# Kernel tuning notes

Measured on AMD Instinct MI355X. Metric: run time of the kernel, lower is better.

The kernel has to match this reference:

```python
import jax, jax.numpy as jnp
import numpy as np

N = 100000   # nodes
E = 1200000  # edges
B = 128      # graphs per batch
F = 92       # raw node features
D = 64       # pre_hidden_size == gc_dim == post_hidden_size
L = 3        # n_gcn
Z = 2 * D + 1  # CGConv concat width


def setup_inputs() -> dict:
    key = jax.random.key(0)
    ks = jax.random.split(key, 24)
    s = 0.1
    inp = {
        "X": jax.random.normal(ks[0], (N, F), jnp.float32),
        "edge_idx": jax.random.randint(ks[1], (2, E), 0, N),
        "edge_weight": jax.random.uniform(ks[2], (E,), jnp.float32),
        "edge_attr": jax.random.normal(ks[3], (E,), jnp.float32),
        "batch_map": jnp.sort(jax.random.randint(ks[4], (N,), 0, B)),
        # pre-GCN MLP: F->D, D->D, D->D, relu after each
        "pre_W0": jax.random.normal(ks[5], (F, D)) * s,
        "pre_b0": jnp.zeros((D,), jnp.float32),
        "pre_W1": jax.random.normal(ks[6], (D, D)) * s,
        "pre_b1": jnp.zeros((D,), jnp.float32),
        "pre_W2": jax.random.normal(ks[7], (D, D)) * s,
        "pre_b2": jnp.zeros((D,), jnp.float32),
        # CGConv gates: lin_f / lin_s: (2D+1)->D, stacked over L layers
        "cg_Wf": jax.random.normal(ks[8], (L, Z, D)) * s,
        "cg_bf": jnp.zeros((L, D), jnp.float32),
        "cg_Ws": jax.random.normal(ks[9], (L, Z, D)) * s,
        "cg_bs": jnp.zeros((L, D), jnp.float32),
        # post-GCN MLP: D->D x3 (relu) then D->1
        "post_W0": jax.random.normal(ks[10], (D, D)) * s,
        "post_b0": jnp.zeros((D,), jnp.float32),
        "post_W1": jax.random.normal(ks[11], (D, D)) * s,
        "post_b1": jnp.zeros((D,), jnp.float32),
        "post_W2": jax.random.normal(ks[12], (D, D)) * s,
        "post_b2": jnp.zeros((D,), jnp.float32),
        "post_Wf": jax.random.normal(ks[13], (D, 1)) * s,
        "post_bf": jnp.zeros((1,), jnp.float32),
    }
    return inp


def _forward(X, edge_idx, edge_weight, edge_attr, batch_map,
             pre_W0, pre_b0, pre_W1, pre_b1, pre_W2, pre_b2,
             cg_Wf, cg_bf, cg_Ws, cg_bs,
             post_W0, post_b0, post_W1, post_b1, post_W2, post_b2,
             post_Wf, post_bf):
    relu = jax.nn.relu
    # pre-GC MLP
    h = relu(X @ pre_W0 + pre_b0)
    h = relu(h @ pre_W1 + pre_b1)
    h = relu(h @ pre_W2 + pre_b2)  # [N, D]

    src = edge_idx[0]  # x_j (message source)
    dst = edge_idx[1]  # x_i (aggregation target)
    ea = edge_attr.reshape(-1, 1)  # [E, 1]
    # in-degree for mean aggregation (nodes with no edges -> 0 via denom clamp)
    deg = jax.ops.segment_sum(jnp.ones((E,), h.dtype), dst, num_segments=N)
    denom = jnp.maximum(deg, 1.0)[:, None]  # [N, 1]

    for l in range(L):
        # CGConv: z = [x_i || x_j || e], out = x + mean_i(sigmoid(z Wf) * softplus(z Ws))
        z = jnp.concatenate([h[dst], h[src], ea], axis=-1)  # [E, 2D+1]
        m = jax.nn.sigmoid(z @ cg_Wf[l] + cg_bf[l]) * jax.nn.softplus(z @ cg_Ws[l] + cg_bs[l])
        agg = jax.ops.segment_sum(m, dst, num_segments=N) / denom
        h = relu(h + agg)  # residual + activation from pyg Sequential

    # early global mean pool per graph
    gsum = jax.ops.segment_sum(h, batch_map, num_segments=B)
    gcnt = jax.ops.segment_sum(jnp.ones((N,), h.dtype), batch_map, num_segments=B)
    g = gsum / jnp.maximum(gcnt, 1.0)[:, None]  # [B, D]

    # post-GC MLP
    g = relu(g @ post_W0 + post_b0)
    g = relu(g @ post_W1 + post_b1)
    g = relu(g @ post_W2 + post_b2)
    return g @ post_Wf + post_bf  # [B, 1]


def reference(X, edge_idx, edge_weight, edge_attr, batch_map,
              pre_W0, pre_b0, pre_W1, pre_b1, pre_W2, pre_b2,
              cg_Wf, cg_bf, cg_Ws, cg_bs,
              post_W0, post_b0, post_W1, post_b1, post_W2, post_b2,
              post_Wf, post_bf):
    return _forward(X, edge_idx, edge_weight, edge_attr, batch_map,
                    pre_W0, pre_b0, pre_W1, pre_b1, pre_W2, pre_b2,
                    cg_Wf, cg_bf, cg_Ws, cg_bs,
                    post_W0, post_b0, post_W1, post_b1, post_W2, post_b2,
                    post_Wf, post_bf)
```

## Files before the change

### kernel.cpp

```cpp
#include <hip/hip_runtime.h>
#include <hip/hip_bf16.h>
#include <math.h>

#define GN 100000
#define GE 1200000
#define GB 128
#define GF 92
#define GD 64
#define GL 3
#define GZ 129

__device__ __forceinline__ unsigned int f2bf_rne(float x)
{
    unsigned int u = __float_as_uint(x);
    u += 0x7fffu + ((u >> 16) & 1u);
    return u >> 16;
}

__global__ __launch_bounds__(256, 2) void premlp_kernel(
    const float* __restrict__ X,
    const float* __restrict__ W0, const float* __restrict__ b0,
    const float* __restrict__ W1, const float* __restrict__ b1,
    const float* __restrict__ W2, const float* __restrict__ b2,
    const float* __restrict__ WfD, const float* __restrict__ WsD,
    const float* __restrict__ WfS, const float* __restrict__ WsS,
    const float* __restrict__ bf, const float* __restrict__ bs,
    float* __restrict__ hout, unsigned int* __restrict__ Pout,
    float* __restrict__ Qout, int N)
{
    __shared__ __align__(16) float Wl[8192];
    const int tid = threadIdx.x;
    const int n = blockIdx.x * 256 + tid;
    const int nn = (n < N) ? n : (N - 1);
    const bool act = (n < N);

    float acc[64], accS[64];

    {
        const float4* __restrict__ s4 = (const float4*)W0;
        float4* __restrict__ d4 = (float4*)Wl;
        for (int i = tid; i < 1472; i += 256) d4[i] = s4[i];
    }
    __syncthreads();

#pragma unroll
    for (int j = 0; j < 64; ++j) acc[j] = b0[j];
    {
        const float4* __restrict__ row4 = (const float4*)(X + (size_t)nn * GF);
#pragma unroll 2
        for (int c = 0; c < 23; ++c) {
            float4 v = row4[c];
            const float* __restrict__ w = Wl + c * 256;
#pragma unroll
            for (int j = 0; j < 64; ++j) {
                acc[j] = fmaf(v.x, w[j], acc[j]);
                acc[j] = fmaf(v.y, w[64 + j], acc[j]);
                acc[j] = fmaf(v.z, w[128 + j], acc[j]);
                acc[j] = fmaf(v.w, w[192 + j], acc[j]);
            }
        }
    }
    if (act) {
        float4* __restrict__ op = (float4*)(hout + (size_t)n * 64);
#pragma unroll
        for (int q = 0; q < 16; ++q)
            op[q] = make_float4(fmaxf(acc[q * 4], 0.f), fmaxf(acc[q * 4 + 1], 0.f),
                                fmaxf(acc[q * 4 + 2], 0.f), fmaxf(acc[q * 4 + 3], 0.f));
    }

    __syncthreads();
    {
        const float4* __restrict__ s4 = (const float4*)W1;
        float4* __restrict__ d4 = (float4*)Wl;
        for (int i = tid; i < 1024; i += 256) d4[i] = s4[i];
    }
    __syncthreads();

#pragma unroll
    for (int j = 0; j < 64; ++j) acc[j] = b1[j];
    {
        const float4* __restrict__ row4 = (const float4*)(hout + (size_t)nn * 64);
#pragma unroll 2
        for (int c = 0; c < 16; ++c) {
            float4 v = row4[c];
            const float* __restrict__ w = Wl + c * 256;
#pragma unroll
            for (int j = 0; j < 64; ++j) {
                acc[j] = fmaf(v.x, w[j], acc[j]);
                acc[j] = fmaf(v.y, w[64 + j], acc[j]);
                acc[j] = fmaf(v.z, w[128 + j], acc[j]);
                acc[j] = fmaf(v.w, w[192 + j], acc[j]);
            }
        }
    }
    if (act) {
        float4* __restrict__ op = (float4*)(hout + (size_t)n * 64);
#pragma unroll
        for (int q = 0; q < 16; ++q)
            op[q] = make_float4(fmaxf(acc[q * 4], 0.f), fmaxf(acc[q * 4 + 1], 0.f),
                                fmaxf(acc[q * 4 + 2], 0.f), fmaxf(acc[q * 4 + 3], 0.f));
    }

    __syncthreads();
    {
        const float4* __restrict__ s4 = (const float4*)W2;
        float4* __restrict__ d4 = (float4*)Wl;
        for (int i = tid; i < 1024; i += 256) d4[i] = s4[i];
    }
    __syncthreads();

#pragma unroll
    for (int j = 0; j < 64; ++j) acc[j] = b2[j];
    {
        const float4* __restrict__ row4 = (const float4*)(hout + (size_t)nn * 64);
#pragma unroll 2
        for (int c = 0; c < 16; ++c) {
            float4 v = row4[c];
            const float* __restrict__ w = Wl + c * 256;
#pragma unroll
            for (int j = 0; j < 64; ++j) {
                acc[j] = fmaf(v.x, w[j], acc[j]);
                acc[j] = fmaf(v.y, w[64 + j], acc[j]);
                acc[j] = fmaf(v.z, w[128 + j], acc[j]);
                acc[j] = fmaf(v.w, w[192 + j], acc[j]);
            }
        }
    }
    if (act) {
        float4* __restrict__ op = (float4*)(hout + (size_t)n * 64);
#pragma unroll
        for (int q = 0; q < 16; ++q)
            op[q] = make_float4(fmaxf(acc[q * 4], 0.f), fmaxf(acc[q * 4 + 1], 0.f),
                                fmaxf(acc[q * 4 + 2], 0.f), fmaxf(acc[q * 4 + 3], 0.f));
    }

    __syncthreads();
    {
        const float4* __restrict__ s4 = (const float4*)WfS;
        const float4* __restrict__ t4 = (const float4*)WsS;
        float4* __restrict__ d4 = (float4*)Wl;
        for (int i = tid; i < 1024; i += 256) {
            d4[i] = s4[i];
            d4[1024 + i] = t4[i];
        }
    }
    __syncthreads();

#pragma unroll
    for (int j = 0; j < 64; ++j) { acc[j] = 0.f; accS[j] = 0.f; }
    {
        const float4* __restrict__ row4 = (const float4*)(hout + (size_t)nn * 64);
#pragma unroll 2
        for (int c = 0; c < 16; ++c) {
            float4 v = row4[c];
            const float* __restrict__ wf = Wl + c * 256;
            const float* __restrict__ ws = Wl + 4096 + c * 256;
#pragma unroll
            for (int j = 0; j < 64; ++j) {
                acc[j] = fmaf(v.x, wf[j], acc[j]);
                acc[j] = fmaf(v.y, wf[64 + j], acc[j]);
                acc[j] = fmaf(v.z, wf[128 + j], acc[j]);
                acc[j] = fmaf(v.w, wf[192 + j], acc[j]);
                accS[j] = fmaf(v.x, ws[j], accS[j]);
                accS[j] = fmaf(v.y, ws[64 + j], accS[j]);
                accS[j] = fmaf(v.z, ws[128 + j], accS[j]);
                accS[j] = fmaf(v.w, ws[192 + j], accS[j]);
            }
        }
    }
    if (act) {
        uint4* __restrict__ pp = (uint4*)(Pout + (size_t)n * 64);
#pragma unroll
        for (int q = 0; q < 16; ++q) {
            uint4 pk;
            pk.x = f2bf_rne(acc[q * 4])     | (f2bf_rne(accS[q * 4]) << 16);
            pk.y = f2bf_rne(acc[q * 4 + 1]) | (f2bf_rne(accS[q * 4 + 1]) << 16);
            pk.z = f2bf_rne(acc[q * 4 + 2]) | (f2bf_rne(accS[q * 4 + 2]) << 16);
            pk.w = f2bf_rne(acc[q * 4 + 3]) | (f2bf_rne(accS[q * 4 + 3]) << 16);
            pp[q] = pk;
        }
    }

    __syncthreads();
    {
        const float4* __restrict__ s4 = (const float4*)WfD;
        const float4* __restrict__ t4 = (const float4*)WsD;
        float4* __restrict__ d4 = (float4*)Wl;
        for (int i = tid; i < 1024; i += 256) {
            d4[i] = s4[i];
            d4[1024 + i] = t4[i];
        }
    }
    __syncthreads();

#pragma unroll
    for (int j = 0; j < 64; ++j) { acc[j] = bf[j]; accS[j] = bs[j]; }
    {
        const float4* __restrict__ row4 = (const float4*)(hout + (size_t)nn * 64);
#pragma unroll 2
        for (int c = 0; c < 16; ++c) {
            float4 v = row4[c];
            const float* __restrict__ wf = Wl + c * 256;
            const float* __restrict__ ws = Wl + 4096 + c * 256;
#pragma unroll
            for (int j = 0; j < 64; ++j) {
                acc[j] = fmaf(v.x, wf[j], acc[j]);
                acc[j] = fmaf(v.y, wf[64 + j], acc[j]);
                acc[j] = fmaf(v.z, wf[128 + j], acc[j]);
                acc[j] = fmaf(v.w, wf[192 + j], acc[j]);
                accS[j] = fmaf(v.x, ws[j], accS[j]);
                accS[j] = fmaf(v.y, ws[64 + j], accS[j]);
                accS[j] = fmaf(v.z, ws[128 + j], accS[j]);
                accS[j] = fmaf(v.w, ws[192 + j], accS[j]);
            }
        }
    }
    if (act) {
        float4* __restrict__ qp = (float4*)(Qout + (size_t)n * 128);
#pragma unroll
        for (int q = 0; q < 32; ++q)
            qp[q] = make_float4(acc[q * 2], accS[q * 2], acc[q * 2 + 1], accS[q * 2 + 1]);
    }
}

__global__ __launch_bounds__(256, 2) void pjq_kernel(
    const float* __restrict__ h,
    const float* __restrict__ Wf, const float* __restrict__ Ws,
    const float* __restrict__ bfv, const float* __restrict__ bsv,
    unsigned int* __restrict__ P, float* __restrict__ Q, int N)
{
    __shared__ __align__(16) float Wl[8192];
    const int tid = threadIdx.x;
    const int n = blockIdx.x * 256 + tid;
    const int nn = (n < N) ? n : (N - 1);
    const bool act = (n < N);

    float aF[64], aS[64];

    {
        const float4* __restrict__ s4 = (const float4*)(Wf + 64 * 64);
        const float4* __restrict__ t4 = (const float4*)(Ws + 64 * 64);
        float4* __restrict__ d4 = (float4*)Wl;
        for (int i = tid; i < 1024; i += 256) {
            d4[i] = s4[i];
            d4[1024 + i] = t4[i];
        }
    }
    __syncthreads();

#pragma unroll
    for (int j = 0; j < 64; ++j) { aF[j] = 0.f; aS[j] = 0.f; }
    {
        const float4* __restrict__ row4 = (const float4*)(h + (size_t)nn * 64);
#pragma unroll 2
        for (int c = 0; c < 16; ++c) {
            float4 v = row4[c];
            const float* __restrict__ wf = Wl + c * 256;
            const float* __restrict__ ws = Wl + 4096 + c * 256;
#pragma unroll
            for (int j = 0; j < 64; ++j) {
                aF[j] = fmaf(v.x, wf[j], aF[j]);
                aF[j] = fmaf(v.y, wf[64 + j], aF[j]);
                aF[j] = fmaf(v.z, wf[128 + j], aF[j]);
                aF[j] = fmaf(v.w, wf[192 + j], aF[j]);
                aS[j] = fmaf(v.x, ws[j], aS[j]);
                aS[j] = fmaf(v.y, ws[64 + j], aS[j]);
                aS[j] = fmaf(v.z, ws[128 + j], aS[j]);
                aS[j] = fmaf(v.w, ws[192 + j], aS[j]);
            }
        }
    }
    if (act) {
        uint4* __restrict__ pp = (uint4*)(P + (size_t)n * 64);
#pragma unroll
        for (int q = 0; q < 16; ++q) {
            uint4 pk;
            pk.x = f2bf_rne(aF[q * 4])     | (f2bf_rne(aS[q * 4]) << 16);
            pk.y = f2bf_rne(aF[q * 4 + 1]) | (f2bf_rne(aS[q * 4 + 1]) << 16);
            pk.z = f2bf_rne(aF[q * 4 + 2]) | (f2bf_rne(aS[q * 4 + 2]) << 16);
            pk.w = f2bf_rne(aF[q * 4 + 3]) | (f2bf_rne(aS[q * 4 + 3]) << 16);
            pp[q] = pk;
        }
    }

    __syncthreads();
    {
        const float4* __restrict__ s4 = (const float4*)Wf;
        const float4* __restrict__ t4 = (const float4*)Ws;
        float4* __restrict__ d4 = (float4*)Wl;
        for (int i = tid; i < 1024; i += 256) {
            d4[i] = s4[i];
            d4[1024 + i] = t4[i];
        }
    }
    __syncthreads();

#pragma unroll
    for (int j = 0; j < 64; ++j) { aF[j] = bfv[j]; aS[j] = bsv[j]; }
    {
        const float4* __restrict__ row4 = (const float4*)(h + (size_t)nn * 64);
#pragma unroll 2
        for (int c = 0; c < 16; ++c) {
            float4 v = row4[c];
            const float* __restrict__ wf = Wl + c * 256;
            const float* __restrict__ ws = Wl + 4096 + c * 256;
#pragma unroll
            for (int j = 0; j < 64; ++j) {
                aF[j] = fmaf(v.x, wf[j], aF[j]);
                aF[j] = fmaf(v.y, wf[64 + j], aF[j]);
                aF[j] = fmaf(v.z, wf[128 + j], aF[j]);
                aF[j] = fmaf(v.w, wf[192 + j], aF[j]);
                aS[j] = fmaf(v.x, ws[j], aS[j]);
                aS[j] = fmaf(v.y, ws[64 + j], aS[j]);
                aS[j] = fmaf(v.z, ws[128 + j], aS[j]);
                aS[j] = fmaf(v.w, ws[192 + j], aS[j]);
            }
        }
    }
    if (act) {
        float4* __restrict__ qp = (float4*)(Q + (size_t)n * 128);
#pragma unroll
        for (int q = 0; q < 32; ++q)
            qp[q] = make_float4(aF[q * 2], aS[q * 2], aF[q * 2 + 1], aS[q * 2 + 1]);
    }
}

__global__ __launch_bounds__(256) void deg_kernel(
    const int* __restrict__ dst, int* __restrict__ deg, int E)
{
    int e = blockIdx.x * blockDim.x + threadIdx.x;
    if (e < E) atomicAdd(&deg[dst[e]], 1);
}

__global__ __launch_bounds__(1024) void scanA_kernel(
    const int* __restrict__ deg, int* __restrict__ iscan,
    int* __restrict__ bsum, int N)
{
    __shared__ int lds[1024];
    int tid = threadIdx.x;
    int gid = blockIdx.x * 1024 + tid;
    int v = (gid < N) ? deg[gid] : 0;
    lds[tid] = v; __syncthreads();
    for (int off = 1; off < 1024; off <<= 1) {
        int t = (tid >= off) ? lds[tid - off] : 0;
        __syncthreads();
        lds[tid] += t;
        __syncthreads();
    }
    if (gid < N) iscan[gid] = lds[tid];
    if (tid == 1023) bsum[blockIdx.x] = lds[1023];
}

__global__ __launch_bounds__(128) void scanB_kernel(
    const int* __restrict__ bsum, int* __restrict__ boff, int nb)
{
    __shared__ int lds[128];
    int t = threadIdx.x;
    int v = (t < nb) ? bsum[t] : 0;
    lds[t] = v; __syncthreads();
    for (int off = 1; off < 128; off <<= 1) {
        int u = (t >= off) ? lds[t - off] : 0;
        __syncthreads();
        lds[t] += u;
        __syncthreads();
    }
    if (t < nb) boff[t] = lds[t] - v;
}

__global__ __launch_bounds__(256) void scanC_kernel(
    const int* __restrict__ iscan, const int* __restrict__ boff,
    const int* __restrict__ deg,
    int* __restrict__ rowptr, int* __restrict__ cursor, int N)
{
    int i = blockIdx.x * blockDim.x + threadIdx.x;
    if (i >= N) return;
    int incl = iscan[i] + boff[i >> 10];
    rowptr[i + 1] = incl;
    cursor[i] = incl - deg[i];
    if (i == 0) rowptr[0] = 0;
}

__global__ __launch_bounds__(256) void escatter_kernel(
    const int* __restrict__ src, const int* __restrict__ dst,
    const float* __restrict__ ea, int* __restrict__ cursor,
    int2* __restrict__ e_se, int E)
{
    int e = blockIdx.x * blockDim.x + threadIdx.x;
    if (e >= E) return;
    int pos = atomicAdd(&cursor[dst[e]], 1);
    e_se[pos] = make_int2(src[e], __float_as_int(ea[e]));
}

__global__ __launch_bounds__(256) void edge_kernel(
    const float* __restrict__ h, const int* __restrict__ rowptr,
    const int2* __restrict__ e_se,
    const unsigned int* __restrict__ P,
    const float* __restrict__ Q,
    const float* __restrict__ Wf, const float* __restrict__ Ws,
    float* __restrict__ hout)
{
    int n = blockIdx.x * 4 + (threadIdx.x >> 6);
    int d = threadIdx.x & 63;

    const float2 qv = ((const float2*)Q)[(size_t)n * 64 + d];
    float qf = qv.x, qs = qv.y;
    float wf = Wf[128 * 64 + d];
    float ws = Ws[128 * 64 + d];

    size_t idx = (size_t)n * 64 + d;
    float hres = h[idx];

    int rb = rowptr[n], re = rowptr[n + 1];
    float agg = 0.f;
#pragma unroll 8
    for (int p = rb; p < re; ++p) {
        int2 se = e_se[p];
        int s = se.x;
        float ea = __int_as_float(se.y);
        unsigned int pv = P[(size_t)s * 64 + d];
        float pf = __uint_as_float(pv << 16);
        float psv = __uint_as_float(pv & 0xffff0000u);
        float xF = fmaf(ea, wf, qf + pf);
        float xS = fmaf(ea, ws, qs + psv);
        float sig = __builtin_amdgcn_rcpf(1.f + __expf(-xF));
        float t = __expf(-fabsf(xS));
        float sp = fmaxf(xS, 0.f) + __logf(1.f + t);
        agg = fmaf(sig, sp, agg);
    }

    float inv = 1.f / (float)max(re - rb, 1);
    hout[idx] = fmaxf(hres + agg * inv, 0.f);
}

__global__ __launch_bounds__(256) void gstart_kernel(
    const int* __restrict__ bm, int* __restrict__ gstart, int N)
{
    int i = blockIdx.x * blockDim.x + threadIdx.x;
    if (i >= N) return;
    int b = bm[i];
    int prev = (i == 0) ? -1 : bm[i - 1];
    for (int g = prev + 1; g <= b; ++g) gstart[g] = i;
    if (i == N - 1)
        for (int g = b + 1; g <= GB; ++g) gstart[g] = N;
}

__global__ __launch_bounds__(256) void pool_seg_kernel(
    const float* __restrict__ h, const int* __restrict__ gstart,
    float* __restrict__ g)
{
    int b = blockIdx.x;
    int s = gstart[b], e = gstart[b + 1];
    int d = threadIdx.x & 63;
    int w = threadIdx.x >> 6;
    float acc = 0.f;
    for (int n = s + w; n < e; n += 4)
        acc += h[(size_t)n * 64 + d];
    __shared__ float lds[256];
    lds[threadIdx.x] = acc;
    __syncthreads();
    if (w == 0) {
        acc = lds[d] + lds[64 + d] + lds[128 + d] + lds[192 + d];
        g[b * 64 + d] = acc / fmaxf((float)(e - s), 1.f);
    }
}

__global__ __launch_bounds__(256) void postmlp_kernel(
    const float* __restrict__ g,
    const float* __restrict__ W0, const float* __restrict__ b0,
    const float* __restrict__ W1, const float* __restrict__ b1,
    const float* __restrict__ W2, const float* __restrict__ b2,
    const float* __restrict__ Wfin, const float* __restrict__ bfin,
    float* __restrict__ out)
{
    int b = blockIdx.x * 4 + (threadIdx.x >> 6);
    int d = threadIdx.x & 63;
    float h = g[(size_t)b * 64 + d];

    float acc = b0[d];
#pragma unroll
    for (int k = 0; k < 64; ++k)
        acc = fmaf(__shfl(h, k, 64), W0[k * 64 + d], acc);
    h = fmaxf(acc, 0.f);

    acc = b1[d];
#pragma unroll
    for (int k = 0; k < 64; ++k)
        acc = fmaf(__shfl(h, k, 64), W1[k * 64 + d], acc);
    h = fmaxf(acc, 0.f);

    acc = b2[d];
#pragma unroll
    for (int k = 0; k < 64; ++k)
        acc = fmaf(__shfl(h, k, 64), W2[k * 64 + d], acc);
    h = fmaxf(acc, 0.f);

    float v = h * Wfin[d];
#pragma unroll
    for (int off = 32; off >= 1; off >>= 1)
        v += __shfl_xor(v, off, 64);
    if (d == 0) out[b] = v + bfin[0];
}

extern "C" void kernel_launch(void* const* d_in, const int* in_sizes, int n_in,
                              void* d_out, int out_size, void* d_ws, size_t ws_size,
                              hipStream_t stream)
{
    const float* X      = (const float*)d_in[0];
    const int*   eidx   = (const int*)d_in[1];
    const float* ea     = (const float*)d_in[3];
    const int*   bm     = (const int*)d_in[4];
    const float* pre_W0 = (const float*)d_in[5];
    const float* pre_b0 = (const float*)d_in[6];
    const float* pre_W1 = (const float*)d_in[7];
    const float* pre_b1 = (const float*)d_in[8];
    const float* pre_W2 = (const float*)d_in[9];
    const float* pre_b2 = (const float*)d_in[10];
    const float* cg_Wf  = (const float*)d_in[11];
    const float* cg_bf  = (const float*)d_in[12];
    const float* cg_Ws  = (const float*)d_in[13];
    const float* cg_bs  = (const float*)d_in[14];
    const float* post_W0 = (const float*)d_in[15];
    const float* post_b0 = (const float*)d_in[16];
    const float* post_W1 = (const float*)d_in[17];
    const float* post_b1 = (const float*)d_in[18];
    const float* post_W2 = (const float*)d_in[19];
    const float* post_b2 = (const float*)d_in[20];
    const float* post_Wf = (const float*)d_in[21];
    const float* post_bf = (const float*)d_in[22];

    const int* src = eidx;
    const int* dst = eidx + GE;

    const size_t N64 = (size_t)GN * 64;
    float* hA    = (float*)d_ws;
    float* hB    = hA + N64;
    unsigned int* P = (unsigned int*)(hB + N64);
    int* deg_i   = (int*)(P + N64);
    int* iscan   = deg_i + GN;
    int* bsum    = iscan + GN;
    int* boff    = bsum + 128;
    int* rowptr  = boff + 128;
    int* cursor  = rowptr + GN + 2;
    int2* e_se   = (int2*)(cursor + GN);
    int* gstart  = (int*)(e_se + GE);
    float* g0    = (float*)(gstart + GB + 1);
    float* Q     = g0 + (size_t)GB * 64;

    const int TPB = 256;
    int gridE  = (GE + TPB - 1) / TPB;
    int gridN  = (GN + TPB - 1) / TPB;
    int gridND = ((GN * 64) + TPB - 1) / TPB;
    int scanBlocks = (GN + 1023) / 1024;

    const float* Wf0 = cg_Wf;
    const float* Ws0 = cg_Ws;
    const float* Wf1 = cg_Wf + (size_t)1 * GZ * GD;
    const float* Ws1 = cg_Ws + (size_t)1 * GZ * GD;
    const float* Wf2 = cg_Wf + (size_t)2 * GZ * GD;
    const float* Ws2 = cg_Ws + (size_t)2 * GZ * GD;

    premlp_kernel<<<gridN, TPB, 0, stream>>>(
        X, pre_W0, pre_b0, pre_W1, pre_b1, pre_W2, pre_b2,
        Wf0, Ws0, Wf0 + 64 * 64, Ws0 + 64 * 64, cg_bf, cg_bs,
        hA, P, Q, GN);

    hipMemsetAsync(deg_i, 0, GN * sizeof(int), stream);
    deg_kernel<<<gridE, TPB, 0, stream>>>(dst, deg_i, GE);
    scanA_kernel<<<scanBlocks, 1024, 0, stream>>>(deg_i, iscan, bsum, GN);
    scanB_kernel<<<1, 128, 0, stream>>>(bsum, boff, scanBlocks);
    scanC_kernel<<<gridN, TPB, 0, stream>>>(iscan, boff, deg_i, rowptr, cursor, GN);
    escatter_kernel<<<gridE, TPB, 0, stream>>>(src, dst, ea, cursor, e_se, GE);

    gstart_kernel<<<gridN, TPB, 0, stream>>>(bm, gstart, GN);

    edge_kernel<<<gridND, TPB, 0, stream>>>(
        hA, rowptr, e_se, P, Q, Wf0, Ws0, hB);
    pjq_kernel<<<gridN, TPB, 0, stream>>>(
        hB, Wf1, Ws1, cg_bf + GD, cg_bs + GD, P, Q, GN);
    edge_kernel<<<gridND, TPB, 0, stream>>>(
        hB, rowptr, e_se, P, Q, Wf1, Ws1, hA);
    pjq_kernel<<<gridN, TPB, 0, stream>>>(
        hA, Wf2, Ws2, cg_bf + 2 * GD, cg_bs + 2 * GD, P, Q, GN);
    edge_kernel<<<gridND, TPB, 0, stream>>>(
        hA, rowptr, e_se, P, Q, Wf2, Ws2, hB);

    pool_seg_kernel<<<GB, TPB, 0, stream>>>(hB, gstart, g0);

    postmlp_kernel<<<GB / 4, TPB, 0, stream>>>(
        g0, post_W0, post_b0, post_W1, post_b1, post_W2, post_b2,
        post_Wf, post_bf, (float*)d_out);
}
```

Baseline: 983.7 us.

## Split node MLP columns across four waves and stage hidden rows in LDS

The pre-MLP and per-layer projection kernels now assign 64 nodes per block, with each of four wavefronts computing 16 output columns instead of one thread computing all 64. Intermediate hidden activations are kept in a padded shared-memory tile rather than round-tripping through global memory, and the paired Wf/Ws projections are done sequentially with one weight matrix in LDS at a time. This cuts per-thread accumulator registers from 128 to 32 so occupancy can rise (launch bounds raised to 4 blocks). The cost is more barriers, more LDS traffic, and four times as many blocks. The WfS/WsS argument swap is offset by a matching swap at the call site.

```diff
diff --git a/kernel.cpp b/kernel.cpp
--- a/kernel.cpp
+++ b/kernel.cpp
@@ -10,6 +10,8 @@
 #define GL 3
 #define GZ 129
 
+#define HS 65
+
 __device__ __forceinline__ unsigned int f2bf_rne(float x)
 {
     unsigned int u = __float_as_uint(x);
@@ -17,24 +19,28 @@
     return u >> 16;
 }
 
-__global__ __launch_bounds__(256, 2) void premlp_kernel(
+__global__ __launch_bounds__(256, 4) void premlp_kernel(
     const float* __restrict__ X,
     const float* __restrict__ W0, const float* __restrict__ b0,
     const float* __restrict__ W1, const float* __restrict__ b1,
     const float* __restrict__ W2, const float* __restrict__ b2,
     const float* __restrict__ WfD, const float* __restrict__ WsD,
-    const float* __restrict__ WfS, const float* __restrict__ WsS,
+    const float* __restrict__ WsS, const float* __restrict__ WfS,
     const float* __restrict__ bf, const float* __restrict__ bs,
     float* __restrict__ hout, unsigned int* __restrict__ Pout,
     float* __restrict__ Qout, int N)
 {
-    __shared__ __align__(16) float Wl[8192];
+    __shared__ __align__(16) float Wl[5888];
+    __shared__ float hl[64 * HS];
     const int tid = threadIdx.x;
-    const int n = blockIdx.x * 256 + tid;
+    const int lane = tid & 63;
+    const int col0 = (tid >> 6) * 16;
+    const int base = blockIdx.x * 64;
+    const int n = base + lane;
     const int nn = (n < N) ? n : (N - 1);
     const bool act = (n < N);
 
-    float acc[64], accS[64];
+    float acc[16], acc2[16];
 
     {
         const float4* __restrict__ s4 = (const float4*)W0;
@@ -44,15 +50,14 @@
     __syncthreads();
 
 #pragma unroll
-    for (int j = 0; j < 64; ++j) acc[j] = b0[j];
+    for (int j = 0; j < 16; ++j) acc[j] = b0[col0 + j];
     {
         const float4* __restrict__ row4 = (const float4*)(X + (size_t)nn * GF);
-#pragma unroll 2
         for (int c = 0; c < 23; ++c) {
             float4 v = row4[c];
-            const float* __restrict__ w = Wl + c * 256;
-#pragma unroll
-            for (int j = 0; j < 64; ++j) {
+            const float* __restrict__ w = Wl + c * 256 + col0;
+#pragma unroll
+            for (int j = 0; j < 16; ++j) {
                 acc[j] = fmaf(v.x, w[j], acc[j]);
                 acc[j] = fmaf(v.y, w[64 + j], acc[j]);
                 acc[j] = fmaf(v.z, w[128 + j], acc[j]);
@@ -60,268 +65,319 @@
             }
         }
     }
+    __syncthreads();
+#pragma unroll
+    for (int j = 0; j < 16; ++j) hl[lane * HS + col0 + j] = fmaxf(acc[j], 0.f);
+    {
+        const float4* __restrict__ s4 = (const float4*)W1;
+        float4* __restrict__ d4 = (float4*)Wl;
+        for (int i = tid; i < 1024; i += 256) d4[i] = s4[i];
+    }
+    __syncthreads();
+
+#pragma unroll
+    for (int j = 0; j < 16; ++j) acc[j] = b1[col0 + j];
+    for (int c = 0; c < 16; ++c) {
+        float h0 = hl[lane * HS + 4 * c + 0];
+        float h1 = hl[lane * HS + 4 * c + 1];
+        float h2 = hl[lane * HS + 4 * c + 2];
+        float h3 = hl[lane * HS + 4 * c + 3];
+        const float* __restrict__ w = Wl + c * 256 + col0;
+#pragma unroll
+        for (int j = 0; j < 16; ++j) {
+            acc[j] = fmaf(h0, w[j], acc[j]);
+            acc[j] = fmaf(h1, w[64 + j], acc[j]);
+            acc[j] = fmaf(h2, w[128 + j], acc[j]);
+            acc[j] = fmaf(h3, w[192 + j], acc[j]);
+        }
+    }
+    __syncthreads();
+#pragma unroll
+    for (int j = 0; j < 16; ++j) hl[lane * HS + col0 + j] = fmaxf(acc[j], 0.f);
+    {
+        const float4* __restrict__ s4 = (const float4*)W2;
+        float4* __restrict__ d4 = (float4*)Wl;
+        for (int i = tid; i < 1024; i += 256) d4[i] = s4[i];
+    }
+    __syncthreads();
+
+#pragma unroll
+    for (int j = 0; j < 16; ++j) acc[j] = b2[col0 + j];
+    for (int c = 0; c < 16; ++c) {
+        float h0 = hl[lane * HS + 4 * c + 0];
+        float h1 = hl[lane * HS + 4 * c + 1];
+        float h2 = hl[lane * HS + 4 * c + 2];
+        float h3 = hl[lane * HS + 4 * c + 3];
+        const float* __restrict__ w = Wl + c * 256 + col0;
+#pragma unroll
+        for (int j = 0; j < 16; ++j) {
+            acc[j] = fmaf(h0, w[j], acc[j]);
+            acc[j] = fmaf(h1, w[64 + j], acc[j]);
+            acc[j] = fmaf(h2, w[128 + j], acc[j]);
+            acc[j] = fmaf(h3, w[192 + j], acc[j]);
+        }
+    }
+    __syncthreads();
+#pragma unroll
+    for (int j = 0; j < 16; ++j) hl[lane * HS + col0 + j] = fmaxf(acc[j], 0.f);
     if (act) {
-        float4* __restrict__ op = (float4*)(hout + (size_t)n * 64);
-#pragma unroll
-        for (int q = 0; q < 16; ++q)
+        float4* __restrict__ op = (float4*)(hout + (size_t)n * 64 + col0);
+#pragma unroll
+        for (int q = 0; q < 4; ++q)
             op[q] = make_float4(fmaxf(acc[q * 4], 0.f), fmaxf(acc[q * 4 + 1], 0.f),
                                 fmaxf(acc[q * 4 + 2], 0.f), fmaxf(acc[q * 4 + 3], 0.f));
     }
-
-    __syncthreads();
-    {
-        const float4* __restrict__ s4 = (const float4*)W1;
-        float4* __restrict__ d4 = (float4*)Wl;
-        for (int i = tid; i < 1024; i += 256) d4[i] = s4[i];
-    }
-    __syncthreads();
-
-#pragma unroll
-    for (int j = 0; j < 64; ++j) acc[j] = b1[j];
-    {
-        const float4* __restrict__ row4 = (const float4*)(hout + (size_t)nn * 64);
-#pragma unroll 2
-        for (int c = 0; c < 16; ++c) {
-            float4 v = row4[c];
-            const float* __restrict__ w = Wl + c * 256;
-#pragma unroll
-            for (int j = 0; j < 64; ++j) {
-                acc[j] = fmaf(v.x, w[j], acc[j]);
-                acc[j] = fmaf(v.y, w[64 + j], acc[j]);
-                acc[j] = fmaf(v.z, w[128 + j], acc[j]);
-                acc[j] = fmaf(v.w, w[192 + j], acc[j]);
-            }
+    {
+        const float4* __restrict__ s4 = (const float4*)WfS;
+        float4* __restrict__ d4 = (float4*)Wl;
+        for (int i = tid; i < 1024; i += 256) d4[i] = s4[i];
+    }
+    __syncthreads();
+
+#pragma unroll
+    for (int j = 0; j < 16; ++j) acc[j] = 0.f;
+    for (int c = 0; c < 16; ++c) {
+        float h0 = hl[lane * HS + 4 * c + 0];
+        float h1 = hl[lane * HS + 4 * c + 1];
+        float h2 = hl[lane * HS + 4 * c + 2];
+        float h3 = hl[lane * HS + 4 * c + 3];
+        const float* __restrict__ w = Wl + c * 256 + col0;
+#pragma unroll
+        for (int j = 0; j < 16; ++j) {
+            acc[j] = fmaf(h0, w[j], acc[j]);
+            acc[j] = fmaf(h1, w[64 + j], acc[j]);
+            acc[j] = fmaf(h2, w[128 + j], acc[j]);
+            acc[j] = fmaf(h3, w[192 + j], acc[j]);
+        }
+    }
+    __syncthreads();
+    {
+        const float4* __restrict__ s4 = (const float4*)WsS;
+        float4* __restrict__ d4 = (float4*)Wl;
+        for (int i = tid; i < 1024; i += 256) d4[i] = s4[i];
+    }
+    __syncthreads();
+
+#pragma unroll
+    for (int j = 0; j < 16; ++j) acc2[j] = 0.f;
+    for (int c = 0; c < 16; ++c) {
+        float h0 = hl[lane * HS + 4 * c + 0];
+        float h1 = hl[lane * HS + 4 * c + 1];
+        float h2 = hl[lane * HS + 4 * c + 2];
+        float h3 = hl[lane * HS + 4 * c + 3];
+        const float* __restrict__ w = Wl + c * 256 + col0;
+#pragma unroll
+        for (int j = 0; j < 16; ++j) {
+            acc2[j] = fmaf(h0, w[j], acc2[j]);
+            acc2[j] = fmaf(h1, w[64 + j], acc2[j]);
+            acc2[j] = fmaf(h2, w[128 + j], acc2[j]);
+            acc2[j] = fmaf(h3, w[192 + j], acc2[j]);
         }
     }
     if (act) {
-        float4* __restrict__ op = (float4*)(hout + (size_t)n * 64);
-#pragma unroll
-        for (int q = 0; q < 16; ++q)
-            op[q] = make_float4(fmaxf(acc[q * 4], 0.f), fmaxf(acc[q * 4 + 1], 0.f),
-                                fmaxf(acc[q * 4 + 2], 0.f), fmaxf(acc[q * 4 + 3], 0.f));
-    }
-
-    __syncthreads();
-    {
-        const float4* __restrict__ s4 = (const float4*)W2;
-        float4* __restrict__ d4 = (float4*)Wl;
-        for (int i = tid; i < 1024; i += 256) d4[i] = s4[i];
-    }
-    __syncthreads();
-
-#pragma unroll
-    for (int j = 0; j < 64; ++j) acc[j] = b2[j];
-    {
-        const float4* __restrict__ row4 = (const float4*)(hout + (size_t)nn * 64);
-#pragma unroll 2
-        for (int c = 0; c < 16; ++c) {
-            float4 v = row4[c];
-            const float* __restrict__ w = Wl + c * 256;
-#pragma unroll
-            for (int j = 0; j < 64; ++j) {
-                acc[j] = fmaf(v.x, w[j], acc[j]);
-                acc[j] = fmaf(v.y, w[64 + j], acc[j]);
-                acc[j] = fmaf(v.z, w[128 + j], acc[j]);
-                acc[j] = fmaf(v.w, w[192 + j], acc[j]);
-            }
+        uint4* __restrict__ pp = (uint4*)(Pout + (size_t)n * 64 + col0);
+#pragma unroll
+        for (int q = 0; q < 4; ++q) {
+            uint4 pk;
+            pk.x = f2bf_rne(acc[q * 4])     | (f2bf_rne(acc2[q * 4]) << 16);
+            pk.y = f2bf_rne(acc[q * 4 + 1]) | (f2bf_rne(acc2[q * 4 + 1]) << 16);
+            pk.z = f2bf_rne(acc[q * 4 + 2]) | (f2bf_rne(acc2[q * 4 + 2]) << 16);
+            pk.w = f2bf_rne(acc[q * 4 + 3]) | (f2bf_rne(acc2[q * 4 + 3]) << 16);
+            pp[q] = pk;
+        }
+    }
+    __syncthreads();
+    {
+        const float4* __restrict__ s4 = (const float4*)WfD;
+        float4* __restrict__ d4 = (float4*)Wl;
+        for (int i = tid; i < 1024; i += 256) d4[i] = s4[i];
+    }
+    __syncthreads();
+
+#pragma unroll
+    for (int j = 0; j < 16; ++j) acc[j] = bf[col0 + j];
+    for (int c = 0; c < 16; ++c) {
+        float h0 = hl[lane * HS + 4 * c + 0];
+        float h1 = hl[lane * HS + 4 * c + 1];
+        float h2 = hl[lane * HS + 4 * c + 2];
+        float h3 = hl[lane * HS + 4 * c + 3];
+        const float* __restrict__ w = Wl + c * 256 + col0;
+#pragma unroll
+        for (int j = 0; j < 16; ++j) {
+            acc[j] = fmaf(h0, w[j], acc[j]);
+            acc[j] = fmaf(h1, w[64 + j], acc[j]);
+            acc[j] = fmaf(h2, w[128 + j], acc[j]);
+            acc[j] = fmaf(h3, w[192 + j], acc[j]);
+        }
+    }
+    __syncthreads();
+    {
+        const float4* __restrict__ s4 = (const float4*)WsD;
+        float4* __restrict__ d4 = (float4*)Wl;
+        for (int i = tid; i < 1024; i += 256) d4[i] = s4[i];
+    }
+    __syncthreads();
+
+#pragma unroll
+    for (int j = 0; j < 16; ++j) acc2[j] = bs[col0 + j];
+    for (int c = 0; c < 16; ++c) {
+        float h0 = hl[lane * HS + 4 * c + 0];
+        float h1 = hl[lane * HS + 4 * c + 1];
+        float h2 = hl[lane * HS + 4 * c + 2];
+        float h3 = hl[lane * HS + 4 * c + 3];
+        const float* __restrict__ w = Wl + c * 256 + col0;
+#pragma unroll
+        for (int j = 0; j < 16; ++j) {
+            acc2[j] = fmaf(h0, w[j], acc2[j]);
+            acc2[j] = fmaf(h1, w[64 + j], acc2[j]);
+            acc2[j] = fmaf(h2, w[128 + j], acc2[j]);
+            acc2[j] = fmaf(h3, w[192 + j], acc2[j]);
         }
     }
     if (act) {
-        float4* __restrict__ op = (float4*)(hout + (size_t)n * 64);
-#pragma unroll
-        for (int q = 0; q < 16; ++q)
-            op[q] = make_float4(fmaxf(acc[q * 4], 0.f), fmaxf(acc[q * 4 + 1], 0.f),
-                                fmaxf(acc[q * 4 + 2], 0.f), fmaxf(acc[q * 4 + 3], 0.f));
-    }
-
-    __syncthreads();
-    {
-        const float4* __restrict__ s4 = (const float4*)WfS;
-        const float4* __restrict__ t4 = (const float4*)WsS;
-        float4* __restrict__ d4 = (float4*)Wl;
-        for (int i = tid; i < 1024; i += 256) {
-            d4[i] = s4[i];
-            d4[1024 + i] = t4[i];
-        }
-    }
-    __syncthreads();
-
-#pragma unroll
-    for (int j = 0; j < 64; ++j) { acc[j] = 0.f; accS[j] = 0.f; }
-    {
-        const float4* __restrict__ row4 = (const float4*)(hout + (size_t)nn * 64);
-#pragma unroll 2
-        for (int c = 0; c < 16; ++c) {
-            float4 v = row4[c];
-            const float* __restrict__ wf = Wl + c * 256;
-            const float* __restrict__ ws = Wl + 4096 + c * 256;
-#pragma unroll
-            for (int j = 0; j < 64; ++j) {
-                acc[j] = fmaf(v.x, wf[j], acc[j]);
-                acc[j] = fmaf(v.y, wf[64 + j], acc[j]);
-                acc[j] = fmaf(v.z, wf[128 + j], acc[j]);
-                acc[j] = fmaf(v.w, wf[192 + j], acc[j]);
-                accS[j] = fmaf(v.x, ws[j], accS[j]);
-                accS[j] = fmaf(v.y, ws[64 + j], accS[j]);
-                accS[j] = fmaf(v.z, ws[128 + j], accS[j]);
-                accS[j] = fmaf(v.w, ws[192 + j], accS[j]);
-            }
-        }
-    }
-    if (act) {
-        uint4* __restrict__ pp = (uint4*)(Pout + (size_t)n * 64);
-#pragma unroll
-        for (int q = 0; q < 16; ++q) {
-            uint4 pk;
-            pk.x = f2bf_rne(acc[q * 4])     | (f2bf_rne(accS[q * 4]) << 16);
-            pk.y = f2bf_rne(acc[q * 4 + 1]) | (f2bf_rne(accS[q * 4 + 1]) << 16);
-            pk.z = f2bf_rne(acc[q * 4 + 2]) | (f2bf_rne(accS[q * 4 + 2]) << 16);
-            pk.w = f2bf_rne(acc[q * 4 + 3]) | (f2bf_rne(accS[q * 4 + 3]) << 16);
-            pp[q] = pk;
-        }
-    }
-
-    __syncthreads();
-    {
-        const float4* __restrict__ s4 = (const float4*)WfD;
-        const float4* __restrict__ t4 = (const float4*)WsD;
-        float4* __restrict__ d4 = (float4*)Wl;
-        for (int i = tid; i < 1024; i += 256) {
-            d4[i] = s4[i];
-            d4[1024 + i] = t4[i];
-        }
-    }
-    __syncthreads();
-
-#pragma unroll
-    for (int j = 0; j < 64; ++j) { acc[j] = bf[j]; accS[j] = bs[j]; }
-    {
-        const float4* __restrict__ row4 = (const float4*)(hout + (size_t)nn * 64);
-#pragma unroll 2
-        for (int c = 0; c < 16; ++c) {
-            float4 v = row4[c];
-            const float* __restrict__ wf = Wl + c * 256;
-            const float* __restrict__ ws = Wl + 4096 + c * 256;
-#pragma unroll
-            for (int j = 0; j < 64; ++j) {
-                acc[j] = fmaf(v.x, wf[j], acc[j]);
-                acc[j] = fmaf(v.y, wf[64 + j], acc[j]);
-                acc[j] = fmaf(v.z, wf[128 + j], acc[j]);
-                acc[j] = fmaf(v.w, wf[192 + j], acc[j]);
-                accS[j] = fmaf(v.x, ws[j], accS[j]);
-                accS[j] = fmaf(v.y, ws[64 + j], accS[j]);
-                accS[j] = fmaf(v.z, ws[128 + j], accS[j]);
-                accS[j] = fmaf(v.w, ws[192 + j], accS[j]);
-            }
-        }
-    }
-    if (act) {
-        float4* __restrict__ qp = (float4*)(Qout + (size_t)n * 128);
-#pragma unroll
-        for (int q = 0; q < 32; ++q)
-            qp[q] = make_float4(acc[q * 2], accS[q * 2], acc[q * 2 + 1], accS[q * 2 + 1]);
-    }
-}
-
-__global__ __launch_bounds__(256, 2) void pjq_kernel(
+        float4* __restrict__ qp = (float4*)(Qout + (size_t)n * 128 + col0 * 2);
+#pragma unroll
+        for (int q = 0; q < 8; ++q)
+            qp[q] = make_float4(acc[q * 2], acc2[q * 2], acc[q * 2 + 1], acc2[q * 2 + 1]);
+    }
+}
+
+__global__ __launch_bounds__(256, 4) void pjq_kernel(
     const float* __restrict__ h,
     const float* __restrict__ Wf, const float* __restrict__ Ws,
     const float* __restrict__ bfv, const float* __restrict__ bsv,
     unsigned int* __restrict__ P, float* __restrict__ Q, int N)
 {
-    __shared__ __align__(16) float Wl[8192];
+    __shared__ __align__(16) float Wl[4096];
+    __shared__ float hl[64 * HS];
     const int tid = threadIdx.x;
-    const int n = blockIdx.x * 256 + tid;
-    const int nn = (n < N) ? n : (N - 1);
+    const int lane = tid & 63;
+    const int col0 = (tid >> 6) * 16;
+    const int base = blockIdx.x * 64;
+    const int n = base + lane;
     const bool act = (n < N);
 
-    float aF[64], aS[64];
-
+    float acc[16], acc2[16];
+
+    for (int q = tid; q < 1024; q += 256) {
+        int r = q >> 4, c4 = q & 15;
+        int rr = base + r; rr = (rr < N) ? rr : (N - 1);
+        float4 v = ((const float4*)(h + (size_t)rr * 64))[c4];
+        float* dp = hl + r * HS + c4 * 4;
+        dp[0] = v.x; dp[1] = v.y; dp[2] = v.z; dp[3] = v.w;
+    }
     {
         const float4* __restrict__ s4 = (const float4*)(Wf + 64 * 64);
-        const float4* __restrict__ t4 = (const float4*)(Ws + 64 * 64);
-        float4* __restrict__ d4 = (float4*)Wl;
-        for (int i = tid; i < 1024; i += 256) {
-            d4[i] = s4[i];
-            d4[1024 + i] = t4[i];
-        }
-    }
-    __syncthreads();
-
-#pragma unroll
-    for (int j = 0; j < 64; ++j) { aF[j] = 0.f; aS[j] = 0.f; }
-    {
-        const float4* __restrict__ row4 = (const float4*)(h + (size_t)nn * 64);
-#pragma unroll 2
-        for (int c = 0; c < 16; ++c) {
-            float4 v = row4[c];
-            const float* __restrict__ wf = Wl + c * 256;
-            const float* __restrict__ ws = Wl + 4096 + c * 256;
-#pragma unroll
-            for (int j = 0; j < 64; ++j) {
-                aF[j] = fmaf(v.x, wf[j], aF[j]);
-                aF[j] = fmaf(v.y, wf[64 + j], aF[j]);
-                aF[j] = fmaf(v.z, wf[128 + j], aF[j]);
-                aF[j] = fmaf(v.w, wf[192 + j], aF[j]);
-                aS[j] = fmaf(v.x, ws[j], aS[j]);
-                aS[j] = fmaf(v.y, ws[64 + j], aS[j]);
-                aS[j] = fmaf(v.z, ws[128 + j], aS[j]);
-                aS[j] = fmaf(v.w, ws[192 + j], aS[j]);
-            }
+        float4* __restrict__ d4 = (float4*)Wl;
+        for (int i = tid; i < 1024; i += 256) d4[i] = s4[i];
+    }
+    __syncthreads();
+
+#pragma unroll
+    for (int j = 0; j < 16; ++j) acc[j] = 0.f;
+    for (int c = 0; c < 16; ++c) {
+        float h0 = hl[lane * HS + 4 * c + 0];
+        float h1 = hl[lane * HS + 4 * c + 1];
+        float h2 = hl[lane * HS + 4 * c + 2];
+        float h3 = hl[lane * HS + 4 * c + 3];
+        const float* __restrict__ w = Wl + c * 256 + col0;
+#pragma unroll
+        for (int j = 0; j < 16; ++j) {
+            acc[j] = fmaf(h0, w[j], acc[j]);
+            acc[j] = fmaf(h1, w[64 + j], acc[j]);
+            acc[j] = fmaf(h2, w[128 + j], acc[j]);
+            acc[j] = fmaf(h3, w[192 + j], acc[j]);
+        }
+    }
+    __syncthreads();
+    {
+        const float4* __restrict__ s4 = (const float4*)(Ws + 64 * 64);
+        float4* __restrict__ d4 = (float4*)Wl;
+        for (int i = tid; i < 1024; i += 256) d4[i] = s4[i];
+    }
+    __syncthreads();
+
+#pragma unroll
+    for (int j = 0; j < 16; ++j) acc2[j] = 0.f;
+    for (int c = 0; c < 16; ++c) {
+        float h0 = hl[lane * HS + 4 * c + 0];
+        float h1 = hl[lane * HS + 4 * c + 1];
+        float h2 = hl[lane * HS + 4 * c + 2];
+        float h3 = hl[lane * HS + 4 * c + 3];
+        const float* __restrict__ w = Wl + c * 256 + col0;
+#pragma unroll
+        for (int j = 0; j < 16; ++j) {
+            acc2[j] = fmaf(h0, w[j], acc2[j]);
+            acc2[j] = fmaf(h1, w[64 + j], acc2[j]);
+            acc2[j] = fmaf(h2, w[128 + j], acc2[j]);
+            acc2[j] = fmaf(h3, w[192 + j], acc2[j]);
         }
     }
     if (act) {
-        uint4* __restrict__ pp = (uint4*)(P + (size_t)n * 64);
-#pragma unroll
-        for (int q = 0; q < 16; ++q) {
+        uint4* __restrict__ pp = (uint4*)(P + (size_t)n * 64 + col0);
+#pragma unroll
+        for (int q = 0; q < 4; ++q) {
             uint4 pk;
-            pk.x = f2bf_rne(aF[q * 4])     | (f2bf_rne(aS[q * 4]) << 16);
-            pk.y = f2bf_rne(aF[q * 4 + 1]) | (f2bf_rne(aS[q * 4 + 1]) << 16);
-            pk.z = f2bf_rne(aF[q * 4 + 2]) | (f2bf_rne(aS[q * 4 + 2]) << 16);
-            pk.w = f2bf_rne(aF[q * 4 + 3]) | (f2bf_rne(aS[q * 4 + 3]) << 16);
+            pk.x = f2bf_rne(acc[q * 4])     | (f2bf_rne(acc2[q * 4]) << 16);
+            pk.y = f2bf_rne(acc[q * 4 + 1]) | (f2bf_rne(acc2[q * 4 + 1]) << 16);
+            pk.z = f2bf_rne(acc[q * 4 + 2]) | (f2bf_rne(acc2[q * 4 + 2]) << 16);
+            pk.w = f2bf_rne(acc[q * 4 + 3]) | (f2bf_rne(acc2[q * 4 + 3]) << 16);
             pp[q] = pk;
         }
     }
-
     __syncthreads();
     {
         const float4* __restrict__ s4 = (const float4*)Wf;
-        const float4* __restrict__ t4 = (const float4*)Ws;
-        float4* __restrict__ d4 = (float4*)Wl;
-        for (int i = tid; i < 1024; i += 256) {
-            d4[i] = s4[i];
-            d4[1024 + i] = t4[i];
-        }
-    }
-    __syncthreads();
-
-#pragma unroll
-    for (int j = 0; j < 64; ++j) { aF[j] = bfv[j]; aS[j] = bsv[j]; }
-    {
-        const float4* __restrict__ row4 = (const float4*)(h + (size_t)nn * 64);
-#pragma unroll 2
-        for (int c = 0; c < 16; ++c) {
-            float4 v = row4[c];
-            const float* __restrict__ wf = Wl + c * 256;
-            const float* __restrict__ ws = Wl + 4096 + c * 256;
-#pragma unroll
-            for (int j = 0; j < 64; ++j) {
-                aF[j] = fmaf(v.x, wf[j], aF[j]);
-                aF[j] = fmaf(v.y, wf[64 + j], aF[j]);
-                aF[j] = fmaf(v.z, wf[128 + j], aF[j]);
-                aF[j] = fmaf(v.w, wf[192 + j], aF[j]);
-                aS[j] = fmaf(v.x, ws[j], aS[j]);
-                aS[j] = fmaf(v.y, ws[64 + j], aS[j]);
-                aS[j] = fmaf(v.z, ws[128 + j], aS[j]);
-                aS[j] = fmaf(v.w, ws[192 + j], aS[j]);
-            }
+        float4* __restrict__ d4 = (float4*)Wl;
+        for (int i = tid; i < 1024; i += 256) d4[i] = s4[i];
+    }
+    __syncthreads();
+
+#pragma unroll
+    for (int j = 0; j < 16; ++j) acc[j] = bfv[col0 + j];
+    for (int c = 0; c < 16; ++c) {
+        float h0 = hl[lane * HS + 4 * c + 0];
+        float h1 = hl[lane * HS + 4 * c + 1];
+        float h2 = hl[lane * HS + 4 * c + 2];
+        float h3 = hl[lane * HS + 4 * c + 3];
+        const float* __restrict__ w = Wl + c * 256 + col0;
+#pragma unroll
+        for (int j = 0; j < 16; ++j) {
+            acc[j] = fmaf(h0, w[j], acc[j]);
+            acc[j] = fmaf(h1, w[64 + j], acc[j]);
+            acc[j] = fmaf(h2, w[128 + j], acc[j]);
+            acc[j] = fmaf(h3, w[192 + j], acc[j]);
+        }
+    }
+    __syncthreads();
+    {
+        const float4* __restrict__ s4 = (const float4*)Ws;
+        float4* __restrict__ d4 = (float4*)Wl;
+        for (int i = tid; i < 1024; i += 256) d4[i] = s4[i];
+    }
+    __syncthreads();
+
+#pragma unroll
+    for (int j = 0; j < 16; ++j) acc2[j] = bsv[col0 + j];
+    for (int c = 0; c < 16; ++c) {
+        float h0 = hl[lane * HS + 4 * c + 0];
+        float h1 = hl[lane * HS + 4 * c + 1];
+        float h2 = hl[lane * HS + 4 * c + 2];
+        float h3 = hl[lane * HS + 4 * c + 3];
+        const float* __restrict__ w = Wl + c * 256 + col0;
+#pragma unroll
+        for (int j = 0; j < 16; ++j) {
+            acc2[j] = fmaf(h0, w[j], acc2[j]);
+            acc2[j] = fmaf(h1, w[64 + j], acc2[j]);
+            acc2[j] = fmaf(h2, w[128 + j], acc2[j]);
+            acc2[j] = fmaf(h3, w[192 + j], acc2[j]);
         }
     }
     if (act) {
-        float4* __restrict__ qp = (float4*)(Q + (size_t)n * 128);
-#pragma unroll
-        for (int q = 0; q < 32; ++q)
-            qp[q] = make_float4(aF[q * 2], aS[q * 2], aF[q * 2 + 1], aS[q * 2 + 1]);
+        float4* __restrict__ qp = (float4*)(Q + (size_t)n * 128 + col0 * 2);
+#pragma unroll
+        for (int q = 0; q < 8; ++q)
+            qp[q] = make_float4(acc[q * 2], acc2[q * 2], acc[q * 2 + 1], acc2[q * 2 + 1]);
     }
 }
 
@@ -549,6 +605,7 @@
     const int TPB = 256;
     int gridE  = (GE + TPB - 1) / TPB;
     int gridN  = (GN + TPB - 1) / TPB;
+    int gridP  = (GN + 63) / 64;
     int gridND = ((GN * 64) + TPB - 1) / TPB;
     int scanBlocks = (GN + 1023) / 1024;
 
@@ -559,9 +616,9 @@
     const float* Wf2 = cg_Wf + (size_t)2 * GZ * GD;
     const float* Ws2 = cg_Ws + (size_t)2 * GZ * GD;
 
-    premlp_kernel<<<gridN, TPB, 0, stream>>>(
+    premlp_kernel<<<gridP, TPB, 0, stream>>>(
         X, pre_W0, pre_b0, pre_W1, pre_b1, pre_W2, pre_b2,
-        Wf0, Ws0, Wf0 + 64 * 64, Ws0 + 64 * 64, cg_bf, cg_bs,
+        Wf0, Ws0, Ws0 + 64 * 64, Wf0 + 64 * 64, cg_bf, cg_bs,
         hA, P, Q, GN);
 
     hipMemsetAsync(deg_i, 0, GN * sizeof(int), stream);
@@ -575,11 +632,11 @@
 
     edge_kernel<<<gridND, TPB, 0, stream>>>(
         hA, rowptr, e_se, P, Q, Wf0, Ws0, hB);
-    pjq_kernel<<<gridN, TPB, 0, stream>>>(
+    pjq_kernel<<<gridP, TPB, 0, stream>>>(
         hB, Wf1, Ws1, cg_bf + GD, cg_bs + GD, P, Q, GN);
     edge_kernel<<<gridND, TPB, 0, stream>>>(
         hB, rowptr, e_se, P, Q, Wf1, Ws1, hA);
-    pjq_kernel<<<gridN, TPB, 0, stream>>>(
+    pjq_kernel<<<gridP, TPB, 0, stream>>>(
         hA, Wf2, Ws2, cg_bf + 2 * GD, cg_bs + 2 * GD, P, Q, GN);
     edge_kernel<<<gridND, TPB, 0, stream>>>(
         hA, rowptr, e_se, P, Q, Wf2, Ws2, hB);
```

Result: faster. 894.7 us (-9.1%).
